# Kernel optimization log

Hardware: AMD Instinct MI355X
Metric: run time of the kernel (lower is better)

## Reference

```python
import jax, jax.numpy as jnp
import numpy as np


def setup_inputs() -> dict:
    key = jax.random.key(0)
    ks = jax.random.split(key, 8)
    B, C, N = 4, 64, 32768
    d = C // 8
    inp = {
        "x": jax.random.normal(ks[0], (B, C, N), dtype=jnp.float32),
        "Wq": jax.random.normal(ks[1], (d, C), dtype=jnp.float32) * 0.1,
        "bq": jax.random.normal(ks[2], (d,), dtype=jnp.float32) * 0.1,
        "Wk": jax.random.normal(ks[3], (d, C), dtype=jnp.float32) * 0.1,
        "bk": jax.random.normal(ks[4], (d,), dtype=jnp.float32) * 0.1,
        "Wv": jax.random.normal(ks[5], (C, C), dtype=jnp.float32) * 0.1,
        "bv": jax.random.normal(ks[6], (C,), dtype=jnp.float32) * 0.1,
        # nn.Parameter(torch.zeros(1)) in the original; nonzero here so the
        # attention branch actually contributes to the output.
        "gamma": jax.random.normal(ks[7], (1,), dtype=jnp.float32) * 0.1,
        "window_size": 512,
        "stride": 256,
        "pooling_factor": 2,
    }
    return inp


def reference(x, Wq, bq, Wk, bk, Wv, bv, gamma, window_size, stride, pooling_factor):
    B, C, N = x.shape
    # conv1x1 projections are pointwise -> apply once on the full signal
    q = jnp.einsum("dc,bcn->bdn", Wq, x) + bq[None, :, None]  # [B, d, N]
    k = jnp.einsum("dc,bcn->bdn", Wk, x) + bk[None, :, None]  # [B, d, N]
    v = jnp.einsum("ec,bcn->ben", Wv, x) + bv[None, :, None]  # [B, C, N]

    starts = jnp.arange(0, N - window_size + 1, stride)              # [W]
    idx = starts[:, None] + jnp.arange(window_size)[None, :]         # [W, ws]

    qw = q[:, :, idx]  # [B, d, W, ws]
    kw = k[:, :, idx]
    vw = v[:, :, idx]  # [B, C, W, ws]
    xw = x[:, :, idx]

    energy = jnp.einsum("bdwi,bdwj->bwij", qw, kw)                   # [B, W, ws, ws]
    attn = jax.nn.softmax(energy, axis=-1)
    # torch: bmm(v, attn^T) -> out[c,i] = sum_j v[c,j] * attn[i,j]
    out_local = jnp.einsum("bcwj,bwij->bcwi", vw, attn)              # [B, C, W, ws]

    contrib = gamma[0] * out_local + xw
    out = jnp.zeros_like(x).at[:, :, idx].add(contrib)               # overlap-add
    counts = jnp.zeros((N,), x.dtype).at[idx].add(1.0)               # overlap count
    out = out / counts[None, None, :]

    P = pooling_factor
    Np = (N // P) * P
    out = out[:, :, :Np].reshape(B, C, N // P, P).max(axis=-1)       # MaxPool1d(P)
    return out
```

## Files before the change

kernel.cpp:

```cpp
#include <hip/hip_runtime.h>
#include <hip/hip_bf16.h>

#define BB 4
#define CC 64
#define DD 8
#define NN 32768
#define WW 512
#define STR 256
#define NWIN 127
#define LOG2E 1.4426950408889634f

typedef short bf16x8 __attribute__((ext_vector_type(8)));
typedef float f32x4 __attribute__((ext_vector_type(4)));
typedef float f32x16 __attribute__((ext_vector_type(16)));

__device__ __forceinline__ unsigned int pack_bf16(float lo, float hi) {
    __hip_bfloat162 h = __float22bfloat162_rn(make_float2(lo, hi));
    unsigned int r; __builtin_memcpy(&r, &h, 4);
    return r;
}
__device__ __forceinline__ unsigned short to_bf16(float f) {
    __hip_bfloat16 h = __float2bfloat16(f);
    unsigned short r; __builtin_memcpy(&r, &h, 2);
    return r;
}
__device__ __forceinline__ float bf2f(unsigned short s) {
    union { unsigned int u; float f; } v; v.u = ((unsigned int)s) << 16;
    return v.f;
}
__device__ __forceinline__ float fast_exp2(float x) {
#if __has_builtin(__builtin_amdgcn_exp2f)
    return __builtin_amdgcn_exp2f(x);
#else
    float r; asm("v_exp_f32 %0, %1" : "=v"(r) : "v"(x)); return r;
#endif
}
__device__ __forceinline__ void plswap(unsigned int &x, unsigned int &y) {
    asm("v_permlane32_swap_b32 %0, %1" : "+v"(x), "+v"(y));
}
__device__ __forceinline__ bf16x8 pack8(float a0, float a1, float a2, float a3,
                                        float a4, float a5, float a6, float a7) {
    union { bf16x8 v; unsigned int u[4]; } r;
    r.u[0] = pack_bf16(a0, a1); r.u[1] = pack_bf16(a2, a3);
    r.u[2] = pack_bf16(a4, a5); r.u[3] = pack_bf16(a6, a7);
    return r.v;
}
__device__ __forceinline__ bf16x8 words4(unsigned int w0, unsigned int w1,
                                         unsigned int w2, unsigned int w3) {
    union { bf16x8 v; unsigned int u[4]; } r;
    r.u[0] = w0; r.u[1] = w1; r.u[2] = w2; r.u[3] = w3;
    return r.v;
}

__global__ __launch_bounds__(256) void qkv_kernel(
    const float* __restrict__ x,
    const float* __restrict__ Wq, const float* __restrict__ bq,
    const float* __restrict__ Wk, const float* __restrict__ bk,
    const float* __restrict__ Wv, const float* __restrict__ bv,
    unsigned short* __restrict__ qout, unsigned short* __restrict__ kout,
    unsigned short* __restrict__ vout)
{
    const int t = threadIdx.x;
    const int lane = t & 63, wv = t >> 6;
    const int a = lane & 15, g = lane >> 4;

    bf16x8 wf[5][2];
    #pragma unroll
    for (int T = 0; T < 5; ++T) {
        const float* wrow;
        float scale = 1.f;
        if (T == 0) {
            if (a < 8) { wrow = Wq + a*CC; scale = LOG2E; }
            else       { wrow = Wk + (a-8)*CC; }
        } else {
            wrow = Wv + ((T-1)*16 + a)*CC;
        }
        #pragma unroll
        for (int h = 0; h < 2; ++h) {
            float4 w0 = *(const float4*)(wrow + h*32 + g*8);
            float4 w1 = *(const float4*)(wrow + h*32 + g*8 + 4);
            wf[T][h] = pack8(w0.x*scale, w0.y*scale, w0.z*scale, w0.w*scale,
                             w1.x*scale, w1.y*scale, w1.z*scale, w1.w*scale);
        }
    }
    f32x4 bias[5];
    {
        const int r = g*4;
        #pragma unroll
        for (int u = 0; u < 4; ++u) {
            int rr = r + u;
            bias[0][u] = (rr < 8) ? bq[rr]*LOG2E : bk[rr-8];
        }
        #pragma unroll
        for (int T = 1; T < 5; ++T)
            #pragma unroll
            for (int u = 0; u < 4; ++u)
                bias[T][u] = bv[(T-1)*16 + r + u];
    }

    const int wave_id = blockIdx.x*4 + wv;
    #pragma unroll 1
    for (int it = 0; it < 2; ++it) {
        const int chunk = wave_id + it*4096;
        const int b = chunk >> 11;
        const int n0 = (chunk & 2047) * 16;
        const int n = n0 + a;
        const float* xcol = x + (size_t)b*CC*NN + n;

        float xv0[8], xv1[8];
        #pragma unroll
        for (int u = 0; u < 8; ++u) xv0[u] = xcol[(size_t)(g*8 + u)*NN];
        #pragma unroll
        for (int u = 0; u < 8; ++u) xv1[u] = xcol[(size_t)(32 + g*8 + u)*NN];
        bf16x8 xb0 = pack8(xv0[0],xv0[1],xv0[2],xv0[3],xv0[4],xv0[5],xv0[6],xv0[7]);
        bf16x8 xb1 = pack8(xv1[0],xv1[1],xv1[2],xv1[3],xv1[4],xv1[5],xv1[6],xv1[7]);

        f32x4 acc[5];
        #pragma unroll
        for (int T = 0; T < 5; ++T) {
            acc[T] = __builtin_amdgcn_mfma_f32_16x16x32_bf16(wf[T][0], xb0, bias[T], 0, 0, 0);
            acc[T] = __builtin_amdgcn_mfma_f32_16x16x32_bf16(wf[T][1], xb1, acc[T], 0, 0, 0);
        }

        {
            unsigned int lo = pack_bf16(acc[0][0], acc[0][1]);
            unsigned int hi = pack_bf16(acc[0][2], acc[0][3]);
            unsigned short* base = ((g < 2) ? qout : kout) + ((size_t)b*NN + n)*8 + (g & 1)*4;
            *(int2*)base = make_int2((int)lo, (int)hi);
        }
        #pragma unroll
        for (int T = 1; T < 5; ++T) {
            #pragma unroll
            for (int u = 0; u < 4; ++u) {
                const int e = (T-1)*16 + g*4 + u;
                vout[((size_t)b*CC + e)*NN + n] = to_bf16(acc[T][u]);
            }
        }
    }
}

__global__ __launch_bounds__(256) void attn_kernel(
    const unsigned short* __restrict__ qg, const unsigned short* __restrict__ kg,
    const unsigned short* __restrict__ vg,
    unsigned short* __restrict__ accE, unsigned short* __restrict__ accO)
{
    __shared__ unsigned short sK[WW][8];
    __shared__ unsigned short sV[2][64][36];
    __shared__ float sInv[4][2][32];
    const int t = threadIdx.x;
    const int lane = t & 63, wv = t >> 6;
    const int l31 = lane & 31, hi = lane >> 5;
    int bid = (blockIdx.x & 7)*127 + (blockIdx.x >> 3);
    const int ih = bid & 1; bid >>= 1;
    const int w = bid % NWIN, b = bid / NWIN;
    const int nwin = STR * w;
    const int i0 = ih*256 + wv*64;

    const unsigned short* qbase = qg + ((size_t)b*NN + nwin + i0)*8;
    const unsigned short* kbase = kg + ((size_t)b*NN + nwin)*8;
    const unsigned short* vsrc  = vg + ((size_t)b*CC + (t >> 2))*NN + nwin + (t & 3)*8;

    #pragma unroll
    for (int m = 0; m < 2; ++m) {
        const int row = m*256 + t;
        *(int4*)&sK[row][0] = *(const int4*)(kbase + (size_t)row*8);
    }
    {
        int4 r = *(const int4*)vsrc;
        unsigned short* dst = &sV[0][t >> 2][(t & 3)*8];
        *(int2*)dst = *(int2*)&r;
        *(int2*)(dst + 4) = *((int2*)&r + 1);
    }

    const bf16x8 zf = {};
    bf16x8 qf[2];
    #pragma unroll
    for (int it = 0; it < 2; ++it) {
        bf16x8 raw = *(const bf16x8*)(qbase + (size_t)(it*32 + l31)*8);
        qf[it] = hi ? zf : raw;
    }

    f32x16 acc[2][2] = {};
    float2 rsum2[2] = {make_float2(0.f,0.f), make_float2(0.f,0.f)};

    __syncthreads();

    for (int jt = 0; jt < 16; ++jt) {
        const int j0 = jt*32;
        const int cur = jt & 1;
        int4 stg;
        if (jt < 15) stg = *(const int4*)(vsrc + j0 + 32);

        bf16x8 kc = *(const bf16x8*)&sK[j0 + l31][0];
        bf16x8 vf[2][2];
        #pragma unroll
        for (int ct = 0; ct < 2; ++ct)
            #pragma unroll
            for (int sl = 0; sl < 2; ++sl) {
                const unsigned short* p = &sV[cur][ct*32 + l31][sl*16 + hi*8];
                union { bf16x8 v; int2 d[2]; } u;
                u.d[0] = *(const int2*)p;
                u.d[1] = *(const int2*)(p + 4);
                vf[ct][sl] = u.v;
            }

        #pragma unroll
        for (int it = 0; it < 2; ++it) {
            const f32x16 z16 = {};
            f32x16 E = __builtin_amdgcn_mfma_f32_32x32x16_bf16(kc, qf[it], z16, 0, 0, 0);
            float p[16];
            #pragma unroll
            for (int r = 0; r < 16; ++r) p[r] = fast_exp2(E[r]);
            float2 s0 = make_float2(p[0],  p[1])  + make_float2(p[2],  p[3]);
            float2 s1 = make_float2(p[4],  p[5])  + make_float2(p[6],  p[7]);
            float2 s2 = make_float2(p[8],  p[9])  + make_float2(p[10], p[11]);
            float2 s3 = make_float2(p[12], p[13]) + make_float2(p[14], p[15]);
            rsum2[it] += (s0 + s1) + (s2 + s3);
            unsigned int wd[8];
            #pragma unroll
            for (int tw = 0; tw < 8; ++tw) wd[tw] = pack_bf16(p[2*tw], p[2*tw+1]);
            unsigned int F0 = wd[0], F2 = wd[2]; plswap(F0, F2);
            unsigned int F1 = wd[1], F3 = wd[3]; plswap(F1, F3);
            unsigned int G0 = wd[4], G2 = wd[6]; plswap(G0, G2);
            unsigned int G1 = wd[5], G3 = wd[7]; plswap(G1, G3);
            bf16x8 pa0 = words4(F0, F1, F2, F3);
            bf16x8 pa1 = words4(G0, G1, G2, G3);
            #pragma unroll
            for (int ct = 0; ct < 2; ++ct) {
                acc[it][ct] = __builtin_amdgcn_mfma_f32_32x32x16_bf16(pa0, vf[ct][0], acc[it][ct], 0, 0, 0);
                acc[it][ct] = __builtin_amdgcn_mfma_f32_32x32x16_bf16(pa1, vf[ct][1], acc[it][ct], 0, 0, 0);
            }
        }

        if (jt < 15) {
            unsigned short* dst = &sV[cur ^ 1][t >> 2][(t & 3)*8];
            *(int2*)dst = *(int2*)&stg;
            *(int2*)(dst + 4) = *((int2*)&stg + 1);
        }
        __syncthreads();
    }

    float rsum[2];
    #pragma unroll
    for (int it = 0; it < 2; ++it) {
        float r = rsum2[it].x + rsum2[it].y;
        r += __shfl_xor(r, 32);
        rsum[it] = r;
    }
    if (lane < 32) {
        sInv[wv][0][lane] = 1.f / rsum[0];
        sInv[wv][1][lane] = 1.f / rsum[1];
    }
    f32x4 invv[2][4];
    #pragma unroll
    for (int it = 0; it < 2; ++it)
        #pragma unroll
        for (int g = 0; g < 4; ++g)
            invv[it][g] = *(const f32x4*)&sInv[wv][it][8*g + 4*hi];

    unsigned short* ob = ((w & 1) ? accO : accE) + (size_t)b*CC*NN + nwin + i0;
    #pragma unroll
    for (int it = 0; it < 2; ++it) {
        #pragma unroll
        for (int ct = 0; ct < 2; ++ct) {
            unsigned short* cbase = ob + (size_t)(ct*32 + l31)*NN + it*32;
            #pragma unroll
            for (int g = 0; g < 4; ++g) {
                float a0 = acc[it][ct][4*g+0] * invv[it][g][0];
                float a1 = acc[it][ct][4*g+1] * invv[it][g][1];
                float a2 = acc[it][ct][4*g+2] * invv[it][g][2];
                float a3 = acc[it][ct][4*g+3] * invv[it][g][3];
                int2 pw = make_int2((int)pack_bf16(a0, a1), (int)pack_bf16(a2, a3));
                *(int2*)(cbase + 8*g + 4*hi) = pw;
            }
        }
    }
}

__global__ __launch_bounds__(256) void final_kernel(
    const float* __restrict__ x,
    const unsigned short* __restrict__ accE, const unsigned short* __restrict__ accO,
    const float* __restrict__ gamma, float* __restrict__ out)
{
    const size_t tid = (size_t)blockIdx.x*256 + threadIdx.x;
    const size_t base = tid*8;
    const int n = (int)(base & (NN-1));
    const float g = gamma[0];

    float xv[8];
    *(float4*)&xv[0] = *(const float4*)&x[base];
    *(float4*)&xv[4] = *(const float4*)&x[base+4];
    int4 aeq = *(const int4*)&accE[base];
    const unsigned int* ae = (const unsigned int*)&aeq;

    float s[8];
    if (n >= STR && n < NN - STR) {
        int4 aoq = *(const int4*)&accO[base];
        const unsigned int* ao = (const unsigned int*)&aoq;
        #pragma unroll
        for (int u = 0; u < 4; ++u) {
            float e0 = bf2f((unsigned short)(ae[u] & 0xffff));
            float e1 = bf2f((unsigned short)(ae[u] >> 16));
            float o0 = bf2f((unsigned short)(ao[u] & 0xffff));
            float o1 = bf2f((unsigned short)(ao[u] >> 16));
            s[2*u]   = fmaf(g, (e0 + o0)*0.5f, xv[2*u]);
            s[2*u+1] = fmaf(g, (e1 + o1)*0.5f, xv[2*u+1]);
        }
    } else {
        #pragma unroll
        for (int u = 0; u < 4; ++u) {
            float e0 = bf2f((unsigned short)(ae[u] & 0xffff));
            float e1 = bf2f((unsigned short)(ae[u] >> 16));
            s[2*u]   = fmaf(g, e0, xv[2*u]);
            s[2*u+1] = fmaf(g, e1, xv[2*u+1]);
        }
    }
    float4 o = make_float4(fmaxf(s[0], s[1]), fmaxf(s[2], s[3]),
                           fmaxf(s[4], s[5]), fmaxf(s[6], s[7]));
    *(float4*)&out[tid*4] = o;
}

extern "C" void kernel_launch(void* const* d_in, const int* in_sizes, int n_in,
                              void* d_out, int out_size, void* d_ws, size_t ws_size,
                              hipStream_t stream)
{
    const float* x    = (const float*)d_in[0];
    const float* Wq   = (const float*)d_in[1];
    const float* bq   = (const float*)d_in[2];
    const float* Wk   = (const float*)d_in[3];
    const float* bk   = (const float*)d_in[4];
    const float* Wv   = (const float*)d_in[5];
    const float* bv   = (const float*)d_in[6];
    const float* gamma= (const float*)d_in[7];

    unsigned short* q    = (unsigned short*)d_ws;
    unsigned short* k    = q + (size_t)BB*NN*DD;
    unsigned short* v    = k + (size_t)BB*NN*DD;
    unsigned short* accE = v + (size_t)BB*CC*NN;
    unsigned short* accO = accE + (size_t)BB*CC*NN;
    float* out = (float*)d_out;

    qkv_kernel<<<1024, 256, 0, stream>>>(x, Wq, bq, Wk, bk, Wv, bv, q, k, v);
    attn_kernel<<<BB*NWIN*2, 256, 0, stream>>>(q, k, v, accE, accO);
    final_kernel<<<BB*CC*NN/8/256, 256, 0, stream>>>(x, accE, accO, gamma, out);
}
```

Baseline: 78.64 us.

## Split attention windows into quarter blocks and software-pipeline QK MFMA

Each block now handles 128 query rows (32 per wave) instead of 256, doubling the grid to four blocks per window, which raises parallelism and lowers per-thread register use. The QK^T MFMA for the next key tile is issued one iteration early so its latency overlaps the exp/pack and PV MFMAs of the current tile. The cost is that each block reloads K and V for half as many queries, doubling K/V global and LDS traffic per window.

```diff
diff --git a/kernel.cpp b/kernel.cpp
--- a/kernel.cpp
+++ b/kernel.cpp
@@ -146,15 +146,15 @@
 {
     __shared__ unsigned short sK[WW][8];
     __shared__ unsigned short sV[2][64][36];
-    __shared__ float sInv[4][2][32];
+    __shared__ float sInv[4][32];
     const int t = threadIdx.x;
     const int lane = t & 63, wv = t >> 6;
     const int l31 = lane & 31, hi = lane >> 5;
-    int bid = (blockIdx.x & 7)*127 + (blockIdx.x >> 3);
-    const int ih = bid & 1; bid >>= 1;
+    int bid = (blockIdx.x & 7)*254 + (blockIdx.x >> 3);
+    const int q2 = bid & 3; bid >>= 2;
     const int w = bid % NWIN, b = bid / NWIN;
     const int nwin = STR * w;
-    const int i0 = ih*256 + wv*64;
+    const int i0 = q2*128 + wv*32;
 
     const unsigned short* qbase = qg + ((size_t)b*NN + nwin + i0)*8;
     const unsigned short* kbase = kg + ((size_t)b*NN + nwin)*8;
@@ -173,25 +173,35 @@
     }
 
     const bf16x8 zf = {};
-    bf16x8 qf[2];
-    #pragma unroll
-    for (int it = 0; it < 2; ++it) {
-        bf16x8 raw = *(const bf16x8*)(qbase + (size_t)(it*32 + l31)*8);
-        qf[it] = hi ? zf : raw;
-    }
-
-    f32x16 acc[2][2] = {};
-    float2 rsum2[2] = {make_float2(0.f,0.f), make_float2(0.f,0.f)};
+    bf16x8 qf;
+    {
+        bf16x8 raw = *(const bf16x8*)(qbase + (size_t)l31*8);
+        qf = hi ? zf : raw;
+    }
+
+    f32x16 acc[2] = {};
+    float2 rsum2 = make_float2(0.f, 0.f);
 
     __syncthreads();
+
+    f32x16 Ecur;
+    {
+        const f32x16 z16 = {};
+        bf16x8 kc = *(const bf16x8*)&sK[l31][0];
+        Ecur = __builtin_amdgcn_mfma_f32_32x32x16_bf16(kc, qf, z16, 0, 0, 0);
+    }
 
     for (int jt = 0; jt < 16; ++jt) {
         const int j0 = jt*32;
         const int cur = jt & 1;
         int4 stg;
         if (jt < 15) stg = *(const int4*)(vsrc + j0 + 32);
-
-        bf16x8 kc = *(const bf16x8*)&sK[j0 + l31][0];
+        f32x16 Enext;
+        if (jt < 15) {
+            const f32x16 z16 = {};
+            bf16x8 kn = *(const bf16x8*)&sK[j0 + 32 + l31][0];
+            Enext = __builtin_amdgcn_mfma_f32_32x32x16_bf16(kn, qf, z16, 0, 0, 0);
+        }
         bf16x8 vf[2][2];
         #pragma unroll
         for (int ct = 0; ct < 2; ++ct)
@@ -203,76 +213,57 @@
                 u.d[1] = *(const int2*)(p + 4);
                 vf[ct][sl] = u.v;
             }
-
-        #pragma unroll
-        for (int it = 0; it < 2; ++it) {
-            const f32x16 z16 = {};
-            f32x16 E = __builtin_amdgcn_mfma_f32_32x32x16_bf16(kc, qf[it], z16, 0, 0, 0);
-            float p[16];
-            #pragma unroll
-            for (int r = 0; r < 16; ++r) p[r] = fast_exp2(E[r]);
-            float2 s0 = make_float2(p[0],  p[1])  + make_float2(p[2],  p[3]);
-            float2 s1 = make_float2(p[4],  p[5])  + make_float2(p[6],  p[7]);
-            float2 s2 = make_float2(p[8],  p[9])  + make_float2(p[10], p[11]);
-            float2 s3 = make_float2(p[12], p[13]) + make_float2(p[14], p[15]);
-            rsum2[it] += (s0 + s1) + (s2 + s3);
-            unsigned int wd[8];
-            #pragma unroll
-            for (int tw = 0; tw < 8; ++tw) wd[tw] = pack_bf16(p[2*tw], p[2*tw+1]);
-            unsigned int F0 = wd[0], F2 = wd[2]; plswap(F0, F2);
-            unsigned int F1 = wd[1], F3 = wd[3]; plswap(F1, F3);
-            unsigned int G0 = wd[4], G2 = wd[6]; plswap(G0, G2);
-            unsigned int G1 = wd[5], G3 = wd[7]; plswap(G1, G3);
-            bf16x8 pa0 = words4(F0, F1, F2, F3);
-            bf16x8 pa1 = words4(G0, G1, G2, G3);
-            #pragma unroll
-            for (int ct = 0; ct < 2; ++ct) {
-                acc[it][ct] = __builtin_amdgcn_mfma_f32_32x32x16_bf16(pa0, vf[ct][0], acc[it][ct], 0, 0, 0);
-                acc[it][ct] = __builtin_amdgcn_mfma_f32_32x32x16_bf16(pa1, vf[ct][1], acc[it][ct], 0, 0, 0);
-            }
-        }
-
+        float p[16];
+        #pragma unroll
+        for (int r = 0; r < 16; ++r) p[r] = fast_exp2(Ecur[r]);
+        float2 s0 = make_float2(p[0],  p[1])  + make_float2(p[2],  p[3]);
+        float2 s1 = make_float2(p[4],  p[5])  + make_float2(p[6],  p[7]);
+        float2 s2 = make_float2(p[8],  p[9])  + make_float2(p[10], p[11]);
+        float2 s3 = make_float2(p[12], p[13]) + make_float2(p[14], p[15]);
+        rsum2 += (s0 + s1) + (s2 + s3);
+        unsigned int wd[8];
+        #pragma unroll
+        for (int tw = 0; tw < 8; ++tw) wd[tw] = pack_bf16(p[2*tw], p[2*tw+1]);
+        unsigned int F0 = wd[0], F2 = wd[2]; plswap(F0, F2);
+        unsigned int F1 = wd[1], F3 = wd[3]; plswap(F1, F3);
+        unsigned int G0 = wd[4], G2 = wd[6]; plswap(G0, G2);
+        unsigned int G1 = wd[5], G3 = wd[7]; plswap(G1, G3);
+        bf16x8 pa0 = words4(F0, F1, F2, F3);
+        bf16x8 pa1 = words4(G0, G1, G2, G3);
+        #pragma unroll
+        for (int ct = 0; ct < 2; ++ct) {
+            acc[ct] = __builtin_amdgcn_mfma_f32_32x32x16_bf16(pa0, vf[ct][0], acc[ct], 0, 0, 0);
+            acc[ct] = __builtin_amdgcn_mfma_f32_32x32x16_bf16(pa1, vf[ct][1], acc[ct], 0, 0, 0);
+        }
         if (jt < 15) {
             unsigned short* dst = &sV[cur ^ 1][t >> 2][(t & 3)*8];
             *(int2*)dst = *(int2*)&stg;
             *(int2*)(dst + 4) = *((int2*)&stg + 1);
         }
         __syncthreads();
-    }
-
-    float rsum[2];
+        Ecur = Enext;
+    }
+
+    float r = rsum2.x + rsum2.y;
+    r += __shfl_xor(r, 32);
+    if (lane < 32) sInv[wv][lane] = 1.f / r;
+    f32x4 invv[4];
     #pragma unroll
-    for (int it = 0; it < 2; ++it) {
-        float r = rsum2[it].x + rsum2[it].y;
-        r += __shfl_xor(r, 32);
-        rsum[it] = r;
-    }
-    if (lane < 32) {
-        sInv[wv][0][lane] = 1.f / rsum[0];
-        sInv[wv][1][lane] = 1.f / rsum[1];
-    }
-    f32x4 invv[2][4];
-    #pragma unroll
-    for (int it = 0; it < 2; ++it)
-        #pragma unroll
-        for (int g = 0; g < 4; ++g)
-            invv[it][g] = *(const f32x4*)&sInv[wv][it][8*g + 4*hi];
+    for (int g = 0; g < 4; ++g)
+        invv[g] = *(const f32x4*)&sInv[wv][8*g + 4*hi];
 
     unsigned short* ob = ((w & 1) ? accO : accE) + (size_t)b*CC*NN + nwin + i0;
     #pragma unroll
-    for (int it = 0; it < 2; ++it) {
-        #pragma unroll
-        for (int ct = 0; ct < 2; ++ct) {
-            unsigned short* cbase = ob + (size_t)(ct*32 + l31)*NN + it*32;
-            #pragma unroll
-            for (int g = 0; g < 4; ++g) {
-                float a0 = acc[it][ct][4*g+0] * invv[it][g][0];
-                float a1 = acc[it][ct][4*g+1] * invv[it][g][1];
-                float a2 = acc[it][ct][4*g+2] * invv[it][g][2];
-                float a3 = acc[it][ct][4*g+3] * invv[it][g][3];
-                int2 pw = make_int2((int)pack_bf16(a0, a1), (int)pack_bf16(a2, a3));
-                *(int2*)(cbase + 8*g + 4*hi) = pw;
-            }
+    for (int ct = 0; ct < 2; ++ct) {
+        unsigned short* cbase = ob + (size_t)(ct*32 + l31)*NN;
+        #pragma unroll
+        for (int g = 0; g < 4; ++g) {
+            float a0 = acc[ct][4*g+0] * invv[g][0];
+            float a1 = acc[ct][4*g+1] * invv[g][1];
+            float a2 = acc[ct][4*g+2] * invv[g][2];
+            float a3 = acc[ct][4*g+3] * invv[g][3];
+            int2 pw = make_int2((int)pack_bf16(a0, a1), (int)pack_bf16(a2, a3));
+            *(int2*)(cbase + 8*g + 4*hi) = pw;
         }
     }
 }
@@ -341,6 +332,6 @@
     float* out = (float*)d_out;
 
     qkv_kernel<<<1024, 256, 0, stream>>>(x, Wq, bq, Wk, bk, Wv, bv, q, k, v);
-    attn_kernel<<<BB*NWIN*2, 256, 0, stream>>>(q, k, v, accE, accO);
+    attn_kernel<<<BB*NWIN*4, 256, 0, stream>>>(q, k, v, accE, accO);
     final_kernel<<<BB*CC*NN/8/256, 256, 0, stream>>>(x, accE, accO, gamma, out);
 }
```

Result: faster. 73.44 us (-6.6%).
